# Kernel optimization log

Measured on AMD Instinct MI355X. Metric: run time of the kernel, lower is better.

## Reference

```python
import jax, jax.numpy as jnp
import numpy as np

F_ = 2048   # feature_size
H_ = 2048   # hidden_size
C_ = 64     # max_children (number of graph nodes)
BN_EPS = 1e-5


def setup_inputs() -> dict:
    key = jax.random.key(0)
    ks = jax.random.split(key, 8)
    s = 0.02
    return {
        "parent_feature": jax.random.normal(ks[0], (1, F_), jnp.float32),
        "child_W": jax.random.normal(ks[1], (C_, F_, F_), jnp.float32) * s,
        "child_b": jnp.zeros((C_, F_), jnp.float32),
        "W1a": jax.random.normal(ks[2], (F_, H_), jnp.float32) * s,
        "b1a": jnp.zeros((H_,), jnp.float32),
        "W1b": jax.random.normal(ks[3], (H_, H_), jnp.float32) * s,
        "b1b": jnp.zeros((H_,), jnp.float32),
        "g1": jnp.ones((H_,), jnp.float32),
        "beta1": jnp.zeros((H_,), jnp.float32),
        "W2a": jax.random.normal(ks[4], (H_, H_), jnp.float32) * s,
        "b2a": jnp.zeros((H_,), jnp.float32),
        "W2b": jax.random.normal(ks[5], (H_, F_), jnp.float32) * s,
        "b2b": jnp.zeros((F_,), jnp.float32),
        "g2": jnp.ones((F_,), jnp.float32),
        "beta2": jnp.zeros((F_,), jnp.float32),
    }


def _batchnorm(x, gamma, beta):
    # BatchNorm1d in training mode: biased batch stats over node dim (axis 0)
    m = x.mean(axis=0)
    v = x.var(axis=0)  # ddof=0, matches torch normalization variance
    return gamma * (x - m) / jnp.sqrt(v + BN_EPS) + beta


def _gin(x, Wa, ba, Wb, bb, recv_mask):
    # completeGraph(C): targets are nodes 1..C-1; each receives sum of ALL nodes
    # (self-loops included). Node 0 receives nothing. eps = 0 (GIN default).
    agg = x.sum(axis=0, keepdims=True) * recv_mask  # [C, D]
    h = x + agg
    return jax.nn.relu(h @ Wa + ba) @ Wb + bb


def reference(parent_feature, child_W, child_b, W1a, b1a, W1b, b1b, g1, beta1,
              W2a, b2a, W2b, b2b, g2, beta2):
    # per-child MLPs: [C, F] node features from the single parent vector
    x = jax.nn.relu(jnp.einsum('f,cfo->co', parent_feature[0], child_W) + child_b)
    recv_mask = (jnp.arange(C_) > 0).astype(x.dtype)[:, None]  # node 0 gets no messages
    x = jax.nn.relu(_gin(x, W1a, b1a, W1b, b1b, recv_mask))
    x = _batchnorm(x, g1, beta1)
    x = jax.nn.relu(_gin(x, W2a, b2a, W2b, b2b, recv_mask))
    x = _batchnorm(x, g2, beta2)
    return x
```

## Files before the change

### kernel.cpp

```cpp
#include <hip/hip_runtime.h>
#include <hip/hip_bf16.h>

#define F_ 2048
#define C_ 64
#define NE (C_ * F_)
#define PGV 8
#define PGM 16

typedef __attribute__((ext_vector_type(4))) float f32x4;

__global__ __launch_bounds__(256) void k_gemv(const float* __restrict__ p,
                                              const float* __restrict__ W,
                                              float* __restrict__ P0) {
    __shared__ float lp[256];
    const int c  = blockIdx.x;
    const int fc = blockIdx.y;
    const int t  = threadIdx.x;
    const int f0 = fc * 256;
    lp[t] = p[f0 + t];
    __syncthreads();

    const float* Wp = W + ((size_t)c << 22) + (size_t)f0 * F_;
    f32x4 aL = (f32x4)(0.f);
    f32x4 aH = (f32x4)(0.f);
#pragma unroll 4
    for (int ff = 0; ff < 256; ++ff) {
        float pv = lp[ff];
        f32x4 wl = __builtin_nontemporal_load((const f32x4*)(Wp + (size_t)ff * F_ + t * 4));
        f32x4 wh = __builtin_nontemporal_load((const f32x4*)(Wp + (size_t)ff * F_ + 1024 + t * 4));
        aL += pv * wl;
        aH += pv * wh;
    }
    float* dst = P0 + (size_t)fc * NE + c * F_;
    *(f32x4*)(dst + t * 4) = aL;
    *(f32x4*)(dst + 1024 + t * 4) = aH;
}

__global__ __launch_bounds__(256) void k_h1(const float* __restrict__ P0,
                                            const float* __restrict__ cb,
                                            float* __restrict__ H1) {
    __shared__ float xs[64 * 10];
    __shared__ float gs[32];
    __shared__ float aggL[8];
    const int t  = threadIdx.x;
    const int o0 = blockIdx.x * 8;
    const int c  = t >> 2;
    const int j  = (t & 3) * 2;

    float2 x = *(const float2*)(cb + c * F_ + o0 + j);
#pragma unroll
    for (int ps = 0; ps < PGV; ++ps) {
        float2 v = *(const float2*)(P0 + (size_t)ps * NE + c * F_ + o0 + j);
        x.x += v.x; x.y += v.y;
    }
    x.x = fmaxf(x.x, 0.f); x.y = fmaxf(x.y, 0.f);
    xs[c * 10 + j + 0] = x.x;
    xs[c * 10 + j + 1] = x.y;
    __syncthreads();

    if (t < 32) {
        const int o = t & 7, cg = t >> 3;
        float s = 0.f;
#pragma unroll
        for (int i = 0; i < 16; ++i) s += xs[(cg * 16 + i) * 10 + o];
        gs[cg * 8 + o] = s;
    }
    __syncthreads();
    if (t < 8) aggL[t] = gs[t] + gs[8 + t] + gs[16 + t] + gs[24 + t];
    __syncthreads();

    float2 r = x;
    if (c > 0) { r.x += aggL[j]; r.y += aggL[j + 1]; }
    *(float2*)(H1 + c * F_ + o0 + j) = r;
}

__global__ __launch_bounds__(256) void k_gemm(const float* __restrict__ Hm,
                                              const float* __restrict__ W,
                                              float* __restrict__ P) {
    __shared__ float Ht[64 * 68];
    __shared__ float Ws[64 * 68];
    const int n0 = blockIdx.x * 64;
    const int k0 = blockIdx.y * 128;
    const int t  = threadIdx.x;
    const int tm4 = (t >> 4) * 4;
    const int tn4 = (t & 15) * 4;

    float4 h0[4]; f32x4 w0[4];
#pragma unroll
    for (int it = 0; it < 4; ++it) {
        int s = t + it * 256;
        h0[it] = *(const float4*)&Hm[(s >> 4) * F_ + k0 + (s & 15) * 4];
        w0[it] = __builtin_nontemporal_load(
            (const f32x4*)&W[(size_t)(k0 + (s >> 4)) * F_ + n0 + (s & 15) * 4]);
    }
#pragma unroll
    for (int it = 0; it < 4; ++it) {
        int s = t + it * 256;
        int m = s >> 4, k4 = (s & 15) * 4;
        Ht[(k4 + 0) * 68 + m] = h0[it].x;
        Ht[(k4 + 1) * 68 + m] = h0[it].y;
        Ht[(k4 + 2) * 68 + m] = h0[it].z;
        Ht[(k4 + 3) * 68 + m] = h0[it].w;
        *(f32x4*)&Ws[(s >> 4) * 68 + (s & 15) * 4] = w0[it];
    }
    __syncthreads();

    float4 h1[4]; f32x4 w1[4];
#pragma unroll
    for (int it = 0; it < 4; ++it) {
        int s = t + it * 256;
        h1[it] = *(const float4*)&Hm[(s >> 4) * F_ + k0 + 64 + (s & 15) * 4];
        w1[it] = __builtin_nontemporal_load(
            (const f32x4*)&W[(size_t)(k0 + 64 + (s >> 4)) * F_ + n0 + (s & 15) * 4]);
    }

    f32x4 acc0 = (f32x4)(0.f), acc1 = (f32x4)(0.f);
    f32x4 acc2 = (f32x4)(0.f), acc3 = (f32x4)(0.f);

#pragma unroll 4
    for (int k = 0; k < 64; ++k) {
        f32x4 a = *(const f32x4*)&Ht[k * 68 + tm4];
        f32x4 b = *(const f32x4*)&Ws[k * 68 + tn4];
        acc0 += a.x * b;
        acc1 += a.y * b;
        acc2 += a.z * b;
        acc3 += a.w * b;
    }
    __syncthreads();

#pragma unroll
    for (int it = 0; it < 4; ++it) {
        int s = t + it * 256;
        int m = s >> 4, k4 = (s & 15) * 4;
        Ht[(k4 + 0) * 68 + m] = h1[it].x;
        Ht[(k4 + 1) * 68 + m] = h1[it].y;
        Ht[(k4 + 2) * 68 + m] = h1[it].z;
        Ht[(k4 + 3) * 68 + m] = h1[it].w;
        *(f32x4*)&Ws[(s >> 4) * 68 + (s & 15) * 4] = w1[it];
    }
    __syncthreads();

#pragma unroll 4
    for (int k = 0; k < 64; ++k) {
        f32x4 a = *(const f32x4*)&Ht[k * 68 + tm4];
        f32x4 b = *(const f32x4*)&Ws[k * 68 + tn4];
        acc0 += a.x * b;
        acc1 += a.y * b;
        acc2 += a.z * b;
        acc3 += a.w * b;
    }

    float* dst = P + (size_t)blockIdx.y * NE + n0 + tn4;
    *(f32x4*)&dst[(tm4 + 0) * F_] = acc0;
    *(f32x4*)&dst[(tm4 + 1) * F_] = acc1;
    *(f32x4*)&dst[(tm4 + 2) * F_] = acc2;
    *(f32x4*)&dst[(tm4 + 3) * F_] = acc3;
}

__global__ __launch_bounds__(256) void k_act(const float* __restrict__ P,
                                             const float* __restrict__ b,
                                             float* __restrict__ T) {
    const int e = (blockIdx.x * 256 + threadIdx.x) * 2;
    const int o = e & (F_ - 1);
    float2 a = *(const float2*)(b + o);
#pragma unroll 8
    for (int ps = 0; ps < PGM; ++ps) {
        float2 v = *(const float2*)(P + (size_t)ps * NE + e);
        a.x += v.x; a.y += v.y;
    }
    a.x = fmaxf(a.x, 0.f); a.y = fmaxf(a.y, 0.f);
    *(float2*)(T + e) = a;
}

__global__ __launch_bounds__(256) void k_bnh(const float* __restrict__ P,
                                             const float* __restrict__ bias,
                                             const float* __restrict__ g,
                                             const float* __restrict__ beta,
                                             float* __restrict__ H) {
    __shared__ float xs[64 * 10];
    __shared__ float gs[32];
    __shared__ float gs2[32];
    __shared__ float mL[8];
    __shared__ float rL[8];
    const int t  = threadIdx.x;
    const int o0 = blockIdx.x * 8;
    const int c  = t >> 2;
    const int j  = (t & 3) * 2;

    float2 x = *(const float2*)(bias + o0 + j);
#pragma unroll 8
    for (int ps = 0; ps < PGM; ++ps) {
        float2 v = *(const float2*)(P + (size_t)ps * NE + c * F_ + o0 + j);
        x.x += v.x; x.y += v.y;
    }
    x.x = fmaxf(x.x, 0.f); x.y = fmaxf(x.y, 0.f);
    xs[c * 10 + j + 0] = x.x;
    xs[c * 10 + j + 1] = x.y;
    __syncthreads();

    if (t < 32) {
        const int o = t & 7, cg = t >> 3;
        float s = 0.f, s2 = 0.f;
#pragma unroll
        for (int i = 0; i < 16; ++i) {
            float v = xs[(cg * 16 + i) * 10 + o];
            s += v; s2 += v * v;
        }
        gs[cg * 8 + o] = s;
        gs2[cg * 8 + o] = s2;
    }
    __syncthreads();
    if (t < 8) {
        float s  = gs[t] + gs[8 + t] + gs[16 + t] + gs[24 + t];
        float s2 = gs2[t] + gs2[8 + t] + gs2[16 + t] + gs2[24 + t];
        float m   = s * (1.f / C_);
        float var = s2 * (1.f / C_) - m * m;
        mL[t] = m;
        rL[t] = 1.f / sqrtf(var + 1e-5f);
    }
    __syncthreads();

    float2 g2v = *(const float2*)(g + o0 + j);
    float2 b2v = *(const float2*)(beta + o0 + j);
    float2 r;
    r.x = (x.x - mL[j + 0]) * rL[j + 0] * g2v.x + b2v.x;
    r.y = (x.y - mL[j + 1]) * rL[j + 1] * g2v.y + b2v.y;
    if (c > 0) {
        r.x += C_ * b2v.x;
        r.y += C_ * b2v.y;
    }
    *(float2*)(H + c * F_ + o0 + j) = r;
}

__global__ __launch_bounds__(256) void k_bn_out(const float* __restrict__ P,
                                                const float* __restrict__ bias,
                                                const float* __restrict__ g,
                                                const float* __restrict__ beta,
                                                float* __restrict__ out) {
    __shared__ float xs[64 * 10];
    __shared__ float gs[32];
    __shared__ float gs2[32];
    __shared__ float mL[8];
    __shared__ float rL[8];
    const int t  = threadIdx.x;
    const int o0 = blockIdx.x * 8;
    const int c  = t >> 2;
    const int j  = (t & 3) * 2;

    float2 x = *(const float2*)(bias + o0 + j);
#pragma unroll 8
    for (int ps = 0; ps < PGM; ++ps) {
        float2 v = *(const float2*)(P + (size_t)ps * NE + c * F_ + o0 + j);
        x.x += v.x; x.y += v.y;
    }
    x.x = fmaxf(x.x, 0.f); x.y = fmaxf(x.y, 0.f);
    xs[c * 10 + j + 0] = x.x;
    xs[c * 10 + j + 1] = x.y;
    __syncthreads();

    if (t < 32) {
        const int o = t & 7, cg = t >> 3;
        float s = 0.f, s2 = 0.f;
#pragma unroll
        for (int i = 0; i < 16; ++i) {
            float v = xs[(cg * 16 + i) * 10 + o];
            s += v; s2 += v * v;
        }
        gs[cg * 8 + o] = s;
        gs2[cg * 8 + o] = s2;
    }
    __syncthreads();
    if (t < 8) {
        float s  = gs[t] + gs[8 + t] + gs[16 + t] + gs[24 + t];
        float s2 = gs2[t] + gs2[8 + t] + gs2[16 + t] + gs2[24 + t];
        float m   = s * (1.f / C_);
        float var = s2 * (1.f / C_) - m * m;
        mL[t] = m;
        rL[t] = 1.f / sqrtf(var + 1e-5f);
    }
    __syncthreads();

    float2 g2v = *(const float2*)(g + o0 + j);
    float2 b2v = *(const float2*)(beta + o0 + j);
    float2 r;
    r.x = (x.x - mL[j + 0]) * rL[j + 0] * g2v.x + b2v.x;
    r.y = (x.y - mL[j + 1]) * rL[j + 1] * g2v.y + b2v.y;
    *(float2*)(out + c * F_ + o0 + j) = r;
}

extern "C" void kernel_launch(void* const* d_in, const int* in_sizes, int n_in,
                              void* d_out, int out_size, void* d_ws, size_t ws_size,
                              hipStream_t stream) {
    const float* p   = (const float*)d_in[0];
    const float* cW  = (const float*)d_in[1];
    const float* cb  = (const float*)d_in[2];
    const float* W1a = (const float*)d_in[3];
    const float* b1a = (const float*)d_in[4];
    const float* W1b = (const float*)d_in[5];
    const float* b1b = (const float*)d_in[6];
    const float* g1  = (const float*)d_in[7];
    const float* be1 = (const float*)d_in[8];
    const float* W2a = (const float*)d_in[9];
    const float* b2a = (const float*)d_in[10];
    const float* W2b = (const float*)d_in[11];
    const float* b2b = (const float*)d_in[12];
    const float* g2  = (const float*)d_in[13];
    const float* be2 = (const float*)d_in[14];
    float* out = (float*)d_out;
    float* ws  = (float*)d_ws;

    float* P  = ws;
    float* H1 = ws + (size_t)16 * NE;
    float* T1 = H1 + NE;
    float* H2 = T1 + NE;
    float* T2 = H2 + NE;

    k_gemv<<<dim3(64, PGV), 256, 0, stream>>>(p, cW, P);
    k_h1<<<256, 256, 0, stream>>>(P, cb, H1);
    k_gemm<<<dim3(32, PGM), 256, 0, stream>>>(H1, W1a, P);
    k_act<<<256, 256, 0, stream>>>(P, b1a, T1);
    k_gemm<<<dim3(32, PGM), 256, 0, stream>>>(T1, W1b, P);
    k_bnh<<<256, 256, 0, stream>>>(P, b1b, g1, be1, H2);
    k_gemm<<<dim3(32, PGM), 256, 0, stream>>>(H2, W2a, P);
    k_act<<<256, 256, 0, stream>>>(P, b2a, T2);
    k_gemm<<<dim3(32, PGM), 256, 0, stream>>>(T2, W2b, P);
    k_bn_out<<<256, 256, 0, stream>>>(P, b2b, g2, be2, out);
}
```

Before: 243.8 us.

## Fuse split-K reduction and activation/batchnorm epilogues into GEMM via last-block counter

Each split-K GEMM now increments a per-column-tile atomic counter after writing its partial. The last block to arrive for a column tile reduces all partials, applies bias and ReLU, and for the batchnorm variants computes the column statistics and normalizes in place. This removes the separate activation and batchnorm kernel launches along with their extra pass over the partial buffer. It adds threadfences, a memset of the counters and a tail in which only the 32 last blocks do the reduction. The gemv loop unroll is also raised from 4 to 8.

```diff
diff --git a/kernel.cpp b/kernel.cpp
--- a/kernel.cpp
+++ b/kernel.cpp
@@ -23,7 +23,7 @@
     const float* Wp = W + ((size_t)c << 22) + (size_t)f0 * F_;
     f32x4 aL = (f32x4)(0.f);
     f32x4 aH = (f32x4)(0.f);
-#pragma unroll 4
+#pragma unroll 8
     for (int ff = 0; ff < 256; ++ff) {
         float pv = lp[ff];
         f32x4 wl = __builtin_nontemporal_load((const f32x4*)(Wp + (size_t)ff * F_ + t * 4));
@@ -74,11 +74,19 @@
     *(float2*)(H1 + c * F_ + o0 + j) = r;
 }
 
-__global__ __launch_bounds__(256) void k_gemm(const float* __restrict__ Hm,
-                                              const float* __restrict__ W,
-                                              float* __restrict__ P) {
-    __shared__ float Ht[64 * 68];
-    __shared__ float Ws[64 * 68];
+template <int MODE>
+__global__ __launch_bounds__(256) void k_gemm_f(const float* __restrict__ Hm,
+                                                const float* __restrict__ W,
+                                                const float* __restrict__ bias,
+                                                const float* __restrict__ g,
+                                                const float* __restrict__ be,
+                                                float* __restrict__ P,
+                                                int* __restrict__ cnt,
+                                                float* __restrict__ Out) {
+    __shared__ float sbuf[2 * 64 * 68 + 128];
+    float* Ht = sbuf;
+    float* Ws = sbuf + 64 * 68;
+    __shared__ int lastS;
     const int n0 = blockIdx.x * 64;
     const int k0 = blockIdx.y * 128;
     const int t  = threadIdx.x;
@@ -121,10 +129,7 @@
     for (int k = 0; k < 64; ++k) {
         f32x4 a = *(const f32x4*)&Ht[k * 68 + tm4];
         f32x4 b = *(const f32x4*)&Ws[k * 68 + tn4];
-        acc0 += a.x * b;
-        acc1 += a.y * b;
-        acc2 += a.z * b;
-        acc3 += a.w * b;
+        acc0 += a.x * b; acc1 += a.y * b; acc2 += a.z * b; acc3 += a.w * b;
     }
     __syncthreads();
 
@@ -144,10 +149,7 @@
     for (int k = 0; k < 64; ++k) {
         f32x4 a = *(const f32x4*)&Ht[k * 68 + tm4];
         f32x4 b = *(const f32x4*)&Ws[k * 68 + tn4];
-        acc0 += a.x * b;
-        acc1 += a.y * b;
-        acc2 += a.z * b;
-        acc3 += a.w * b;
+        acc0 += a.x * b; acc1 += a.y * b; acc2 += a.z * b; acc3 += a.w * b;
     }
 
     float* dst = P + (size_t)blockIdx.y * NE + n0 + tn4;
@@ -155,64 +157,48 @@
     *(f32x4*)&dst[(tm4 + 1) * F_] = acc1;
     *(f32x4*)&dst[(tm4 + 2) * F_] = acc2;
     *(f32x4*)&dst[(tm4 + 3) * F_] = acc3;
-}
-
-__global__ __launch_bounds__(256) void k_act(const float* __restrict__ P,
-                                             const float* __restrict__ b,
-                                             float* __restrict__ T) {
-    const int e = (blockIdx.x * 256 + threadIdx.x) * 2;
-    const int o = e & (F_ - 1);
-    float2 a = *(const float2*)(b + o);
-#pragma unroll 8
-    for (int ps = 0; ps < PGM; ++ps) {
-        float2 v = *(const float2*)(P + (size_t)ps * NE + e);
-        a.x += v.x; a.y += v.y;
-    }
-    a.x = fmaxf(a.x, 0.f); a.y = fmaxf(a.y, 0.f);
-    *(float2*)(T + e) = a;
-}
-
-__global__ __launch_bounds__(256) void k_bnh(const float* __restrict__ P,
-                                             const float* __restrict__ bias,
-                                             const float* __restrict__ g,
-                                             const float* __restrict__ beta,
-                                             float* __restrict__ H) {
-    __shared__ float xs[64 * 10];
-    __shared__ float gs[32];
-    __shared__ float gs2[32];
-    __shared__ float mL[8];
-    __shared__ float rL[8];
-    const int t  = threadIdx.x;
-    const int o0 = blockIdx.x * 8;
-    const int c  = t >> 2;
-    const int j  = (t & 3) * 2;
-
-    float2 x = *(const float2*)(bias + o0 + j);
-#pragma unroll 8
-    for (int ps = 0; ps < PGM; ++ps) {
-        float2 v = *(const float2*)(P + (size_t)ps * NE + c * F_ + o0 + j);
-        x.x += v.x; x.y += v.y;
-    }
-    x.x = fmaxf(x.x, 0.f); x.y = fmaxf(x.y, 0.f);
-    xs[c * 10 + j + 0] = x.x;
-    xs[c * 10 + j + 1] = x.y;
-    __syncthreads();
-
-    if (t < 32) {
-        const int o = t & 7, cg = t >> 3;
+
+    __threadfence();
+    __syncthreads();
+    if (t == 0) lastS = (atomicAdd(&cnt[blockIdx.x], 1) == PGM - 1);
+    __syncthreads();
+    if (!lastS) return;
+    __threadfence();
+
+    f32x4 v[4];
+#pragma unroll
+    for (int i = 0; i < 4; ++i) {
+        int s  = t + i * 256;
+        int c  = s >> 4;
+        int nl = (s & 15) * 4;
+        f32x4 a = *(const f32x4*)&bias[n0 + nl];
+#pragma unroll
+        for (int ps = 0; ps < PGM; ++ps)
+            a += *(const f32x4*)&P[(size_t)ps * NE + c * F_ + n0 + nl];
+        a.x = fmaxf(a.x, 0.f); a.y = fmaxf(a.y, 0.f);
+        a.z = fmaxf(a.z, 0.f); a.w = fmaxf(a.w, 0.f);
+        v[i] = a;
+        if (MODE == 0)
+            *(f32x4*)&Out[c * F_ + n0 + nl] = a;
+    }
+    if (MODE == 0) return;
+
+    float* xs = sbuf;
+    float* mL = sbuf + 64 * 68;
+    float* rL = sbuf + 64 * 68 + 64;
+#pragma unroll
+    for (int i = 0; i < 4; ++i) {
+        int s = t + i * 256;
+        *(f32x4*)&xs[(s >> 4) * 68 + (s & 15) * 4] = v[i];
+    }
+    __syncthreads();
+    if (t < 64) {
         float s = 0.f, s2 = 0.f;
 #pragma unroll
-        for (int i = 0; i < 16; ++i) {
-            float v = xs[(cg * 16 + i) * 10 + o];
-            s += v; s2 += v * v;
+        for (int c = 0; c < C_; ++c) {
+            float x = xs[c * 68 + t];
+            s += x; s2 += x * x;
         }
-        gs[cg * 8 + o] = s;
-        gs2[cg * 8 + o] = s2;
-    }
-    __syncthreads();
-    if (t < 8) {
-        float s  = gs[t] + gs[8 + t] + gs[16 + t] + gs[24 + t];
-        float s2 = gs2[t] + gs2[8 + t] + gs2[16 + t] + gs2[24 + t];
         float m   = s * (1.f / C_);
         float var = s2 * (1.f / C_) - m * m;
         mL[t] = m;
@@ -220,72 +206,22 @@
     }
     __syncthreads();
 
-    float2 g2v = *(const float2*)(g + o0 + j);
-    float2 b2v = *(const float2*)(beta + o0 + j);
-    float2 r;
-    r.x = (x.x - mL[j + 0]) * rL[j + 0] * g2v.x + b2v.x;
-    r.y = (x.y - mL[j + 1]) * rL[j + 1] * g2v.y + b2v.y;
-    if (c > 0) {
-        r.x += C_ * b2v.x;
-        r.y += C_ * b2v.y;
-    }
-    *(float2*)(H + c * F_ + o0 + j) = r;
-}
-
-__global__ __launch_bounds__(256) void k_bn_out(const float* __restrict__ P,
-                                                const float* __restrict__ bias,
-                                                const float* __restrict__ g,
-                                                const float* __restrict__ beta,
-                                                float* __restrict__ out) {
-    __shared__ float xs[64 * 10];
-    __shared__ float gs[32];
-    __shared__ float gs2[32];
-    __shared__ float mL[8];
-    __shared__ float rL[8];
-    const int t  = threadIdx.x;
-    const int o0 = blockIdx.x * 8;
-    const int c  = t >> 2;
-    const int j  = (t & 3) * 2;
-
-    float2 x = *(const float2*)(bias + o0 + j);
-#pragma unroll 8
-    for (int ps = 0; ps < PGM; ++ps) {
-        float2 v = *(const float2*)(P + (size_t)ps * NE + c * F_ + o0 + j);
-        x.x += v.x; x.y += v.y;
-    }
-    x.x = fmaxf(x.x, 0.f); x.y = fmaxf(x.y, 0.f);
-    xs[c * 10 + j + 0] = x.x;
-    xs[c * 10 + j + 1] = x.y;
-    __syncthreads();
-
-    if (t < 32) {
-        const int o = t & 7, cg = t >> 3;
-        float s = 0.f, s2 = 0.f;
-#pragma unroll
-        for (int i = 0; i < 16; ++i) {
-            float v = xs[(cg * 16 + i) * 10 + o];
-            s += v; s2 += v * v;
-        }
-        gs[cg * 8 + o] = s;
-        gs2[cg * 8 + o] = s2;
-    }
-    __syncthreads();
-    if (t < 8) {
-        float s  = gs[t] + gs[8 + t] + gs[16 + t] + gs[24 + t];
-        float s2 = gs2[t] + gs2[8 + t] + gs2[16 + t] + gs2[24 + t];
-        float m   = s * (1.f / C_);
-        float var = s2 * (1.f / C_) - m * m;
-        mL[t] = m;
-        rL[t] = 1.f / sqrtf(var + 1e-5f);
-    }
-    __syncthreads();
-
-    float2 g2v = *(const float2*)(g + o0 + j);
-    float2 b2v = *(const float2*)(beta + o0 + j);
-    float2 r;
-    r.x = (x.x - mL[j + 0]) * rL[j + 0] * g2v.x + b2v.x;
-    r.y = (x.y - mL[j + 1]) * rL[j + 1] * g2v.y + b2v.y;
-    *(float2*)(out + c * F_ + o0 + j) = r;
+#pragma unroll
+    for (int i = 0; i < 4; ++i) {
+        int s  = t + i * 256;
+        int c  = s >> 4;
+        int nl = (s & 15) * 4;
+        f32x4 g4 = *(const f32x4*)&g[n0 + nl];
+        f32x4 b4 = *(const f32x4*)&be[n0 + nl];
+        f32x4 r;
+        r.x = (v[i].x - mL[nl + 0]) * rL[nl + 0] * g4.x + b4.x;
+        r.y = (v[i].y - mL[nl + 1]) * rL[nl + 1] * g4.y + b4.y;
+        r.z = (v[i].z - mL[nl + 2]) * rL[nl + 2] * g4.z + b4.z;
+        r.w = (v[i].w - mL[nl + 3]) * rL[nl + 3] * g4.w + b4.w;
+        if (MODE == 1 && c > 0)
+            r += (float)C_ * b4;
+        *(f32x4*)&Out[c * F_ + n0 + nl] = r;
+    }
 }
 
 extern "C" void kernel_launch(void* const* d_in, const int* in_sizes, int n_in,
@@ -314,15 +250,14 @@
     float* T1 = H1 + NE;
     float* H2 = T1 + NE;
     float* T2 = H2 + NE;
+    int*   cnt = (int*)(T2 + NE);
+
+    hipMemsetAsync(cnt, 0, 4 * 32 * sizeof(int), stream);
 
     k_gemv<<<dim3(64, PGV), 256, 0, stream>>>(p, cW, P);
     k_h1<<<256, 256, 0, stream>>>(P, cb, H1);
-    k_gemm<<<dim3(32, PGM), 256, 0, stream>>>(H1, W1a, P);
-    k_act<<<256, 256, 0, stream>>>(P, b1a, T1);
-    k_gemm<<<dim3(32, PGM), 256, 0, stream>>>(T1, W1b, P);
-    k_bnh<<<256, 256, 0, stream>>>(P, b1b, g1, be1, H2);
-    k_gemm<<<dim3(32, PGM), 256, 0, stream>>>(H2, W2a, P);
-    k_act<<<256, 256, 0, stream>>>(P, b2a, T2);
-    k_gemm<<<dim3(32, PGM), 256, 0, stream>>>(T2, W2b, P);
-    k_bn_out<<<256, 256, 0, stream>>>(P, b2b, g2, be2, out);
-}
+    k_gemm_f<0><<<dim3(32, PGM), 256, 0, stream>>>(H1, W1a, b1a, nullptr, nullptr, P, cnt +  0, T1);
+    k_gemm_f<1><<<dim3(32, PGM), 256, 0, stream>>>(T1, W1b, b1b, g1, be1,         P, cnt + 32, H2);
+    k_gemm_f<0><<<dim3(32, PGM), 256, 0, stream>>>(H2, W2a, b2a, nullptr, nullptr, P, cnt + 64, T2);
+    k_gemm_f<2><<<dim3(32, PGM), 256, 0, stream>>>(T2, W2b, b2b, g2, be2,         P, cnt + 96, out);
+}
```

Result: slower. 455.9 us (+87.0%).
